# Performance work log

Measured on AMD Instinct MI355X. Metric: run time of the kernel, lower is better.

The kernel has to match this reference:

```python
import jax, jax.numpy as jnp
import numpy as np

TOP_K = 8


def setup_inputs() -> dict:
    key = jax.random.key(0)
    k1, k2 = jax.random.split(key)
    B, S, D, E = 4, 4096, 2048, 64
    x = jax.random.normal(k1, (B, S, D), dtype=jnp.float32)
    # nn.Linear(d_model, n_experts): weight [E, D], bias [E]
    W = jax.random.normal(k2, (E, D), dtype=jnp.float32) * (1.0 / np.sqrt(D))
    b = jnp.zeros((E,), dtype=jnp.float32)
    return {"x": x, "W": W, "b": b}


def reference(x, W, b):
    # logits: [B, S, E] = x @ W^T + b
    logits = jnp.einsum("bsd,ed->bse", x, W) + b
    scores = jax.nn.sigmoid(logits)                      # [B, S, E]
    B, S, E = scores.shape
    flat = scores.reshape(B * S, E)                      # tokens x experts
    top_w, top_idx = jax.lax.top_k(flat, TOP_K)          # [B*S, k]
    return top_w.reshape(B, S, TOP_K), top_idx.reshape(B, S, TOP_K)
```

## Files before the change

kernel.cpp:

```cpp
#include <hip/hip_runtime.h>
#include <math.h>

#define TOKENS 16384
#define DMODEL 2048
#define NEXP   64
#define TOPK   8
#define BM     64
#define BK     32
#define PAD    4

__global__ __launch_bounds__(256) void router_gemm(
    const float* __restrict__ x, const float* __restrict__ W,
    float* __restrict__ part, int kchunk)
{
    __shared__ float xsT[BK][BM + PAD];
    __shared__ float wsT[BK][NEXP + PAD];

    const int tid = threadIdx.x;
    const int kq  = tid & 7;
    const int row = tid >> 3;
    const int ty  = tid >> 4;
    const int tx  = tid & 15;
    const size_t tokBase = (size_t)blockIdx.x * BM;
    const int    kc      = blockIdx.y;
    const size_t kbase   = (size_t)kc * (size_t)kchunk;

    double accd[4][4];
    float  accf[4][4];
#pragma unroll
    for (int i = 0; i < 4; ++i)
#pragma unroll
        for (int j = 0; j < 4; ++j) { accd[i][j] = 0.0; accf[i][j] = 0.0f; }

    for (int k0 = 0; k0 < kchunk; k0 += BK) {
        const size_t koff = kbase + (size_t)k0 + kq * 4;
        const float4 xa = *(const float4*)(x + (tokBase + row) * DMODEL + koff);
        const float4 xb = *(const float4*)(x + (tokBase + row + 32) * DMODEL + koff);
        const float4 wa = *(const float4*)(W + (size_t)row * DMODEL + koff);
        const float4 wb = *(const float4*)(W + (size_t)(row + 32) * DMODEL + koff);
        __syncthreads();
        xsT[kq * 4 + 0][row] = xa.x; xsT[kq * 4 + 1][row] = xa.y;
        xsT[kq * 4 + 2][row] = xa.z; xsT[kq * 4 + 3][row] = xa.w;
        xsT[kq * 4 + 0][row + 32] = xb.x; xsT[kq * 4 + 1][row + 32] = xb.y;
        xsT[kq * 4 + 2][row + 32] = xb.z; xsT[kq * 4 + 3][row + 32] = xb.w;
        wsT[kq * 4 + 0][row] = wa.x; wsT[kq * 4 + 1][row] = wa.y;
        wsT[kq * 4 + 2][row] = wa.z; wsT[kq * 4 + 3][row] = wa.w;
        wsT[kq * 4 + 0][row + 32] = wb.x; wsT[kq * 4 + 1][row + 32] = wb.y;
        wsT[kq * 4 + 2][row + 32] = wb.z; wsT[kq * 4 + 3][row + 32] = wb.w;
        __syncthreads();

#pragma unroll
        for (int kk = 0; kk < BK; ++kk) {
            const float4 a = *(const float4*)(&xsT[kk][ty * 4]);
            const float4 b = *(const float4*)(&wsT[kk][tx * 4]);
            const float av[4] = {a.x, a.y, a.z, a.w};
            const float bv[4] = {b.x, b.y, b.z, b.w};
#pragma unroll
            for (int i = 0; i < 4; ++i)
#pragma unroll
                for (int j = 0; j < 4; ++j)
                    accf[i][j] = fmaf(av[i], bv[j], accf[i][j]);
            if ((kk & 15) == 15) {
#pragma unroll
                for (int i = 0; i < 4; ++i)
#pragma unroll
                    for (int j = 0; j < 4; ++j) {
                        accd[i][j] += (double)accf[i][j];
                        accf[i][j] = 0.0f;
                    }
            }
        }
    }

#pragma unroll
    for (int i = 0; i < 4; ++i) {
        const size_t tok = tokBase + ty * 4 + i;
        float4 o;
        o.x = (float)accd[i][0]; o.y = (float)accd[i][1];
        o.z = (float)accd[i][2]; o.w = (float)accd[i][3];
        *(float4*)(part + ((size_t)kc * TOKENS + tok) * NEXP + tx * 4) = o;
    }
}

__global__ __launch_bounds__(256) void router_reduce_topk(
    const float* __restrict__ part, const float* __restrict__ bias,
    float* __restrict__ out_w, float* __restrict__ out_i, int ksplit)
{
    const int lane = threadIdx.x & 63;
    const int wid  = threadIdx.x >> 6;
    const size_t t = (size_t)blockIdx.x * 4 + wid;

    double vd = (double)bias[lane];
    for (int kc = 0; kc < ksplit; ++kc)
        vd += (double)part[((size_t)kc * TOKENS + t) * NEXP + lane];
    float v = (float)vd;

    const int myi = lane;
    float bv = 0.0f; int bi = 0;
#pragma unroll
    for (int r = 0; r < TOPK; ++r) {
        float mv = v; int mi = myi;
#pragma unroll
        for (int off = 32; off > 0; off >>= 1) {
            const float ov = __shfl_xor(mv, off, 64);
            const int   oi = __shfl_xor(mi, off, 64);
            if (ov > mv || (ov == mv && oi < mi)) { mv = ov; mi = oi; }
        }
        if (lane == r)  { bv = mv; bi = mi; }
        if (myi == mi)  { v = -INFINITY; }
    }

    if (lane < TOPK) {
        out_w[t * TOPK + lane] = 1.0f / (1.0f + expf(-bv));
        out_i[t * TOPK + lane] = (float)bi;
    }
}

extern "C" void kernel_launch(void* const* d_in, const int* in_sizes, int n_in,
                              void* d_out, int out_size, void* d_ws, size_t ws_size,
                              hipStream_t stream) {
    const float* x    = (const float*)d_in[0];
    const float* W    = (const float*)d_in[1];
    const float* bias = (const float*)d_in[2];
    float* out_w = (float*)d_out;
    float* out_i = (float*)d_out + (size_t)TOKENS * TOPK;
    float* part  = (float*)d_ws;

    const size_t per = (size_t)TOKENS * NEXP * sizeof(float);
    int ksplit = 8;
    while (ksplit > 1 && ws_size < (size_t)ksplit * per) ksplit >>= 1;
    const int kchunk = DMODEL / ksplit;

    dim3 grid(TOKENS / BM, ksplit);
    router_gemm<<<grid, 256, 0, stream>>>(x, W, part, kchunk);
    router_reduce_topk<<<TOKENS / 4, 256, 0, stream>>>(part, bias, out_w, out_i, ksplit);
}
```

Baseline: 234.6 us.

## Prefetch next K tile into registers and store shared tiles row-major with float4

Shared tiles are now stored k-contiguous per row, so each thread writes one float4 instead of sixteen scalar transposed stores. The inner product reads four float4 per operand per 4-k group. The next tile's global loads are issued right after the barrier, so they overlap with the FMA loop on the current tile. In exchange the kernel holds more live registers, and the row-major float4 reads with a 36-float stride may cause LDS bank conflicts.

Result: slower. 284.8 us (+21.4%).

```diff
diff --git a/kernel.cpp b/kernel.cpp
--- a/kernel.cpp
+++ b/kernel.cpp
@@ -7,14 +7,14 @@
 #define TOPK   8
 #define BM     64
 #define BK     32
-#define PAD    4
+#define BKP    36
 
 __global__ __launch_bounds__(256) void router_gemm(
     const float* __restrict__ x, const float* __restrict__ W,
     float* __restrict__ part, int kchunk)
 {
-    __shared__ float xsT[BK][BM + PAD];
-    __shared__ float wsT[BK][NEXP + PAD];
+    __shared__ float xs[BM][BKP];
+    __shared__ float ws[NEXP][BKP];
 
     const int tid = threadIdx.x;
     const int kq  = tid & 7;
@@ -32,35 +32,47 @@
 #pragma unroll
         for (int j = 0; j < 4; ++j) { accd[i][j] = 0.0; accf[i][j] = 0.0f; }
 
-    for (int k0 = 0; k0 < kchunk; k0 += BK) {
-        const size_t koff = kbase + (size_t)k0 + kq * 4;
-        const float4 xa = *(const float4*)(x + (tokBase + row) * DMODEL + koff);
-        const float4 xb = *(const float4*)(x + (tokBase + row + 32) * DMODEL + koff);
-        const float4 wa = *(const float4*)(W + (size_t)row * DMODEL + koff);
-        const float4 wb = *(const float4*)(W + (size_t)(row + 32) * DMODEL + koff);
+    const int ntiles = kchunk / BK;
+
+    size_t koff = kbase + kq * 4;
+    float4 xa = *(const float4*)(x + (tokBase + row) * DMODEL + koff);
+    float4 xb = *(const float4*)(x + (tokBase + row + 32) * DMODEL + koff);
+    float4 wa = *(const float4*)(W + (size_t)row * DMODEL + koff);
+    float4 wb = *(const float4*)(W + (size_t)(row + 32) * DMODEL + koff);
+
+    for (int t = 0; t < ntiles; ++t) {
         __syncthreads();
-        xsT[kq * 4 + 0][row] = xa.x; xsT[kq * 4 + 1][row] = xa.y;
-        xsT[kq * 4 + 2][row] = xa.z; xsT[kq * 4 + 3][row] = xa.w;
-        xsT[kq * 4 + 0][row + 32] = xb.x; xsT[kq * 4 + 1][row + 32] = xb.y;
-        xsT[kq * 4 + 2][row + 32] = xb.z; xsT[kq * 4 + 3][row + 32] = xb.w;
-        wsT[kq * 4 + 0][row] = wa.x; wsT[kq * 4 + 1][row] = wa.y;
-        wsT[kq * 4 + 2][row] = wa.z; wsT[kq * 4 + 3][row] = wa.w;
-        wsT[kq * 4 + 0][row + 32] = wb.x; wsT[kq * 4 + 1][row + 32] = wb.y;
-        wsT[kq * 4 + 2][row + 32] = wb.z; wsT[kq * 4 + 3][row + 32] = wb.w;
+        *(float4*)(&xs[row     ][kq * 4]) = xa;
+        *(float4*)(&xs[row + 32][kq * 4]) = xb;
+        *(float4*)(&ws[row     ][kq * 4]) = wa;
+        *(float4*)(&ws[row + 32][kq * 4]) = wb;
         __syncthreads();
 
+        if (t + 1 < ntiles) {
+            koff = kbase + (size_t)(t + 1) * BK + kq * 4;
+            xa = *(const float4*)(x + (tokBase + row) * DMODEL + koff);
+            xb = *(const float4*)(x + (tokBase + row + 32) * DMODEL + koff);
+            wa = *(const float4*)(W + (size_t)row * DMODEL + koff);
+            wb = *(const float4*)(W + (size_t)(row + 32) * DMODEL + koff);
+        }
+
 #pragma unroll
-        for (int kk = 0; kk < BK; ++kk) {
-            const float4 a = *(const float4*)(&xsT[kk][ty * 4]);
-            const float4 b = *(const float4*)(&wsT[kk][tx * 4]);
-            const float av[4] = {a.x, a.y, a.z, a.w};
-            const float bv[4] = {b.x, b.y, b.z, b.w};
+        for (int g = 0; g < BK / 4; ++g) {
+            float a[16], b[16];
 #pragma unroll
             for (int i = 0; i < 4; ++i)
+                *(float4*)(&a[i * 4]) = *(const float4*)(&xs[ty * 4 + i][g * 4]);
 #pragma unroll
-                for (int j = 0; j < 4; ++j)
-                    accf[i][j] = fmaf(av[i], bv[j], accf[i][j]);
-            if ((kk & 15) == 15) {
+            for (int j = 0; j < 4; ++j)
+                *(float4*)(&b[j * 4]) = *(const float4*)(&ws[tx * 4 + j][g * 4]);
+#pragma unroll
+            for (int c = 0; c < 4; ++c)
+#pragma unroll
+                for (int i = 0; i < 4; ++i)
+#pragma unroll
+                    for (int j = 0; j < 4; ++j)
+                        accf[i][j] = fmaf(a[i * 4 + c], b[j * 4 + c], accf[i][j]);
+            if ((g & 3) == 3) {
 #pragma unroll
                 for (int i = 0; i < 4; ++i)
 #pragma unroll
```

## Read x directly from global memory and prefetch W tiles into registers

Applied to the files above, without the earlier changes.

The x tile is no longer staged through shared memory. Each thread now loads its own four token rows straight from global memory as float4, and only W is kept in LDS. The next W tile is loaded into registers while the current tile is computed, and the double-precision flush now happens once per 32-wide k tile instead of every 16. This removes LDS write traffic for x and overlaps the W global loads with compute, but x is now fetched redundantly by the 16 threads sharing a ty row, which relies on cache hits. The longer fp32 partial sum also changes numerical accumulation slightly.

After: 279.7 us. 19.2% more time.

```diff
diff --git a/kernel.cpp b/kernel.cpp
--- a/kernel.cpp
+++ b/kernel.cpp
@@ -7,14 +7,13 @@
 #define TOPK   8
 #define BM     64
 #define BK     32
-#define PAD    4
+#define WPAD   4
 
 __global__ __launch_bounds__(256) void router_gemm(
     const float* __restrict__ x, const float* __restrict__ W,
     float* __restrict__ part, int kchunk)
 {
-    __shared__ float xsT[BK][BM + PAD];
-    __shared__ float wsT[BK][NEXP + PAD];
+    __shared__ float wsT[BK][NEXP + WPAD];
 
     const int tid = threadIdx.x;
     const int kq  = tid & 7;
@@ -25,6 +24,11 @@
     const int    kc      = blockIdx.y;
     const size_t kbase   = (size_t)kc * (size_t)kchunk;
 
+    const float* xr0 = x + (tokBase + ty * 4 + 0) * DMODEL + kbase;
+    const float* xr1 = x + (tokBase + ty * 4 + 1) * DMODEL + kbase;
+    const float* xr2 = x + (tokBase + ty * 4 + 2) * DMODEL + kbase;
+    const float* xr3 = x + (tokBase + ty * 4 + 3) * DMODEL + kbase;
+
     double accd[4][4];
     float  accf[4][4];
 #pragma unroll
@@ -32,44 +36,60 @@
 #pragma unroll
         for (int j = 0; j < 4; ++j) { accd[i][j] = 0.0; accf[i][j] = 0.0f; }
 
-    for (int k0 = 0; k0 < kchunk; k0 += BK) {
-        const size_t koff = kbase + (size_t)k0 + kq * 4;
-        const float4 xa = *(const float4*)(x + (tokBase + row) * DMODEL + koff);
-        const float4 xb = *(const float4*)(x + (tokBase + row + 32) * DMODEL + koff);
-        const float4 wa = *(const float4*)(W + (size_t)row * DMODEL + koff);
-        const float4 wb = *(const float4*)(W + (size_t)(row + 32) * DMODEL + koff);
+    const int ntiles = kchunk / BK;
+
+    const float* wp = W + (size_t)row * DMODEL + kbase + kq * 4;
+    float4 wa = *(const float4*)(wp);
+    float4 wb = *(const float4*)(wp + (size_t)32 * DMODEL);
+
+    for (int t = 0; t < ntiles; ++t) {
         __syncthreads();
-        xsT[kq * 4 + 0][row] = xa.x; xsT[kq * 4 + 1][row] = xa.y;
-        xsT[kq * 4 + 2][row] = xa.z; xsT[kq * 4 + 3][row] = xa.w;
-        xsT[kq * 4 + 0][row + 32] = xb.x; xsT[kq * 4 + 1][row + 32] = xb.y;
-        xsT[kq * 4 + 2][row + 32] = xb.z; xsT[kq * 4 + 3][row + 32] = xb.w;
         wsT[kq * 4 + 0][row] = wa.x; wsT[kq * 4 + 1][row] = wa.y;
         wsT[kq * 4 + 2][row] = wa.z; wsT[kq * 4 + 3][row] = wa.w;
         wsT[kq * 4 + 0][row + 32] = wb.x; wsT[kq * 4 + 1][row + 32] = wb.y;
         wsT[kq * 4 + 2][row + 32] = wb.z; wsT[kq * 4 + 3][row + 32] = wb.w;
         __syncthreads();
 
+        if (t + 1 < ntiles) {
+            wp += BK;
+            wa = *(const float4*)(wp);
+            wb = *(const float4*)(wp + (size_t)32 * DMODEL);
+        }
+
+        const int kb = t * BK;
 #pragma unroll
-        for (int kk = 0; kk < BK; ++kk) {
-            const float4 a = *(const float4*)(&xsT[kk][ty * 4]);
-            const float4 b = *(const float4*)(&wsT[kk][tx * 4]);
-            const float av[4] = {a.x, a.y, a.z, a.w};
-            const float bv[4] = {b.x, b.y, b.z, b.w};
+        for (int g = 0; g < BK / 4; ++g) {
+            float4 xv0 = *(const float4*)(xr0 + kb + g * 4);
+            float4 xv1 = *(const float4*)(xr1 + kb + g * 4);
+            float4 xv2 = *(const float4*)(xr2 + kb + g * 4);
+            float4 xv3 = *(const float4*)(xr3 + kb + g * 4);
+            float4 b0 = *(const float4*)(&wsT[g * 4 + 0][tx * 4]);
+            float4 b1 = *(const float4*)(&wsT[g * 4 + 1][tx * 4]);
+            float4 b2 = *(const float4*)(&wsT[g * 4 + 2][tx * 4]);
+            float4 b3 = *(const float4*)(&wsT[g * 4 + 3][tx * 4]);
+            const float a[4][4] = {{xv0.x, xv0.y, xv0.z, xv0.w},
+                                   {xv1.x, xv1.y, xv1.z, xv1.w},
+                                   {xv2.x, xv2.y, xv2.z, xv2.w},
+                                   {xv3.x, xv3.y, xv3.z, xv3.w}};
+            const float b[4][4] = {{b0.x, b0.y, b0.z, b0.w},
+                                   {b1.x, b1.y, b1.z, b1.w},
+                                   {b2.x, b2.y, b2.z, b2.w},
+                                   {b3.x, b3.y, b3.z, b3.w}};
 #pragma unroll
-            for (int i = 0; i < 4; ++i)
-#pragma unroll
-                for (int j = 0; j < 4; ++j)
-                    accf[i][j] = fmaf(av[i], bv[j], accf[i][j]);
-            if ((kk & 15) == 15) {
+            for (int c = 0; c < 4; ++c)
 #pragma unroll
                 for (int i = 0; i < 4; ++i)
 #pragma unroll
-                    for (int j = 0; j < 4; ++j) {
-                        accd[i][j] += (double)accf[i][j];
-                        accf[i][j] = 0.0f;
-                    }
+                    for (int j = 0; j < 4; ++j)
+                        accf[i][j] = fmaf(a[i][c], b[c][j], accf[i][j]);
+        }
+#pragma unroll
+        for (int i = 0; i < 4; ++i)
+#pragma unroll
+            for (int j = 0; j < 4; ++j) {
+                accd[i][j] += (double)accf[i][j];
+                accf[i][j] = 0.0f;
             }
-        }
     }
 
 #pragma unroll
```

## Replace FP32 SIMT router GEMM with split-fp16 MFMA using pre-swizzled weights

Applied to the files above, without the earlier changes.

Moves the router GEMM from scalar FMA on LDS tiles to 16x16x32 fp16 MFMA instructions. Each operand is split into high and low fp16 halves, and three MFMAs per step approximate fp32 accuracy. A new kernel converts W into the split fp16 form in MFMA fragment order, and x is read directly from global memory without LDS staging. The split-K factor is fixed at 4. The workspace size check is dropped, and there is some risk of top-k mismatches from reduced precision and fp16 range limits on the low parts.

New measurement: 232.1 us. No clear change (-1.0%).

```diff
diff --git a/kernel.cpp b/kernel.cpp
--- a/kernel.cpp
+++ b/kernel.cpp
@@ -5,80 +5,100 @@
 #define DMODEL 2048
 #define NEXP   64
 #define TOPK   8
-#define BM     64
-#define BK     32
-#define PAD    4
+#define KSPLIT 4
+#define KCHUNK (DMODEL / KSPLIT)
+#define NKS    (KCHUNK / 32)
 
-__global__ __launch_bounds__(256) void router_gemm(
-    const float* __restrict__ x, const float* __restrict__ W,
-    float* __restrict__ part, int kchunk)
+typedef _Float16 half8 __attribute__((ext_vector_type(8)));
+typedef float    f32x4 __attribute__((ext_vector_type(4)));
+
+
+__global__ __launch_bounds__(64) void w_convert(
+    const float* __restrict__ W, _Float16* __restrict__ wh,
+    _Float16* __restrict__ wl)
 {
-    __shared__ float xsT[BK][BM + PAD];
-    __shared__ float wsT[BK][NEXP + PAD];
+    const int lane = threadIdx.x;
+    const int nt   = blockIdx.x & 3;
+    const int ks   = blockIdx.x >> 2;
+    const int n    = nt * 16 + (lane & 15);
+    const int k0   = ks * 32 + (lane >> 4) * 8;
+    const size_t base = ((size_t)(nt * 64 + ks) * 64 + lane) * 8;
+#pragma unroll
+    for (int j = 0; j < 8; ++j) {
+        const float w = W[(size_t)n * DMODEL + k0 + j];
+        const _Float16 h = (_Float16)w;
+        wh[base + j] = h;
+        wl[base + j] = (_Float16)(w - (float)h);
+    }
+}
 
-    const int tid = threadIdx.x;
-    const int kq  = tid & 7;
-    const int row = tid >> 3;
-    const int ty  = tid >> 4;
-    const int tx  = tid & 15;
-    const size_t tokBase = (size_t)blockIdx.x * BM;
-    const int    kc      = blockIdx.y;
-    const size_t kbase   = (size_t)kc * (size_t)kchunk;
+__global__ __launch_bounds__(256) void router_gemm_mfma(
+    const float* __restrict__ x, const _Float16* __restrict__ wh,
+    const _Float16* __restrict__ wl, float* __restrict__ part)
+{
+    const int lane = threadIdx.x & 63;
+    const int wid  = threadIdx.x >> 6;
+    const int kc   = blockIdx.y;
+    const size_t tokBase = (size_t)blockIdx.x * 64 + wid * 16;
+    const int m    = lane & 15;
+    const int quad = lane >> 4;
 
-    double accd[4][4];
-    float  accf[4][4];
+    const float* xrow = x + (tokBase + m) * DMODEL + (size_t)kc * KCHUNK + quad * 8;
+
+    f32x4 C[4];
+    double accd[16];
 #pragma unroll
-    for (int i = 0; i < 4; ++i)
+    for (int nt = 0; nt < 4; ++nt) { C[nt] = (f32x4)0.0f; }
 #pragma unroll
-        for (int j = 0; j < 4; ++j) { accd[i][j] = 0.0; accf[i][j] = 0.0f; }
+    for (int i = 0; i < 16; ++i) accd[i] = 0.0;
 
-    for (int k0 = 0; k0 < kchunk; k0 += BK) {
-        const size_t koff = kbase + (size_t)k0 + kq * 4;
-        const float4 xa = *(const float4*)(x + (tokBase + row) * DMODEL + koff);
-        const float4 xb = *(const float4*)(x + (tokBase + row + 32) * DMODEL + koff);
-        const float4 wa = *(const float4*)(W + (size_t)row * DMODEL + koff);
-        const float4 wb = *(const float4*)(W + (size_t)(row + 32) * DMODEL + koff);
-        __syncthreads();
-        xsT[kq * 4 + 0][row] = xa.x; xsT[kq * 4 + 1][row] = xa.y;
-        xsT[kq * 4 + 2][row] = xa.z; xsT[kq * 4 + 3][row] = xa.w;
-        xsT[kq * 4 + 0][row + 32] = xb.x; xsT[kq * 4 + 1][row + 32] = xb.y;
-        xsT[kq * 4 + 2][row + 32] = xb.z; xsT[kq * 4 + 3][row + 32] = xb.w;
-        wsT[kq * 4 + 0][row] = wa.x; wsT[kq * 4 + 1][row] = wa.y;
-        wsT[kq * 4 + 2][row] = wa.z; wsT[kq * 4 + 3][row] = wa.w;
-        wsT[kq * 4 + 0][row + 32] = wb.x; wsT[kq * 4 + 1][row + 32] = wb.y;
-        wsT[kq * 4 + 2][row + 32] = wb.z; wsT[kq * 4 + 3][row + 32] = wb.w;
-        __syncthreads();
+    for (int ks = 0; ks < NKS; ++ks) {
+        float xv[8];
+        *(float4*)(&xv[0]) = *(const float4*)(xrow + ks * 32);
+        *(float4*)(&xv[4]) = *(const float4*)(xrow + ks * 32 + 4);
+        half8 ah, al;
+#pragma unroll
+        for (int j = 0; j < 8; ++j) {
+            const _Float16 h = (_Float16)xv[j];
+            ah[j] = h;
+            al[j] = (_Float16)(xv[j] - (float)h);
+        }
+        const int gks = kc * NKS + ks;
+        half8 bh[4], bl[4];
+#pragma unroll
+        for (int nt = 0; nt < 4; ++nt) {
+            const size_t fb = ((size_t)(nt * 64 + gks) * 64 + lane) * 8;
+            bh[nt] = *(const half8*)(wh + fb);
+            bl[nt] = *(const half8*)(wl + fb);
+        }
+#pragma unroll
+        for (int nt = 0; nt < 4; ++nt)
+            C[nt] = __builtin_amdgcn_mfma_f32_16x16x32_f16(ah, bh[nt], C[nt], 0, 0, 0);
+#pragma unroll
+        for (int nt = 0; nt < 4; ++nt)
+            C[nt] = __builtin_amdgcn_mfma_f32_16x16x32_f16(al, bh[nt], C[nt], 0, 0, 0);
+#pragma unroll
+        for (int nt = 0; nt < 4; ++nt)
+            C[nt] = __builtin_amdgcn_mfma_f32_16x16x32_f16(ah, bl[nt], C[nt], 0, 0, 0);
 
+        if ((ks & 3) == 3) {
 #pragma unroll
-        for (int kk = 0; kk < BK; ++kk) {
-            const float4 a = *(const float4*)(&xsT[kk][ty * 4]);
-            const float4 b = *(const float4*)(&wsT[kk][tx * 4]);
-            const float av[4] = {a.x, a.y, a.z, a.w};
-            const float bv[4] = {b.x, b.y, b.z, b.w};
+            for (int nt = 0; nt < 4; ++nt) {
 #pragma unroll
-            for (int i = 0; i < 4; ++i)
-#pragma unroll
-                for (int j = 0; j < 4; ++j)
-                    accf[i][j] = fmaf(av[i], bv[j], accf[i][j]);
-            if ((kk & 15) == 15) {
-#pragma unroll
-                for (int i = 0; i < 4; ++i)
-#pragma unroll
-                    for (int j = 0; j < 4; ++j) {
-                        accd[i][j] += (double)accf[i][j];
-                        accf[i][j] = 0.0f;
-                    }
+                for (int r = 0; r < 4; ++r) accd[nt * 4 + r] += (double)C[nt][r];
+                C[nt] = (f32x4)0.0f;
             }
         }
     }
 
 #pragma unroll
-    for (int i = 0; i < 4; ++i) {
-        const size_t tok = tokBase + ty * 4 + i;
-        float4 o;
-        o.x = (float)accd[i][0]; o.y = (float)accd[i][1];
-        o.z = (float)accd[i][2]; o.w = (float)accd[i][3];
-        *(float4*)(part + ((size_t)kc * TOKENS + tok) * NEXP + tx * 4) = o;
+    for (int r = 0; r < 4; ++r) {
+        const size_t tok = tokBase + quad * 4 + r;
+#pragma unroll
+        for (int nt = 0; nt < 4; ++nt) {
+            part[((size_t)kc * TOKENS + tok) * NEXP + nt * 16 + m] =
+                (float)accd[nt * 4 + r];
+        }
     }
 }
 
@@ -124,14 +144,14 @@
     const float* bias = (const float*)d_in[2];
     float* out_w = (float*)d_out;
     float* out_i = (float*)d_out + (size_t)TOKENS * TOPK;
-    float* part  = (float*)d_ws;
 
-    const size_t per = (size_t)TOKENS * NEXP * sizeof(float);
-    int ksplit = 8;
-    while (ksplit > 1 && ws_size < (size_t)ksplit * per) ksplit >>= 1;
-    const int kchunk = DMODEL / ksplit;
+    float*    part = (float*)d_ws;
+    _Float16* wh   = (_Float16*)((char*)d_ws +
+                       (size_t)KSPLIT * TOKENS * NEXP * sizeof(float));
+    _Float16* wl   = wh + (size_t)NEXP * DMODEL;
 
-    dim3 grid(TOKENS / BM, ksplit);
-    router_gemm<<<grid, 256, 0, stream>>>(x, W, part, kchunk);
-    router_reduce_topk<<<TOKENS / 4, 256, 0, stream>>>(part, bias, out_w, out_i, ksplit);
+    w_convert<<<256, 64, 0, stream>>>(W, wh, wl);
+    dim3 grid(TOKENS / 64, KSPLIT);
+    router_gemm_mfma<<<grid, 256, 0, stream>>>(x, wh, wl, part);
+    router_reduce_topk<<<TOKENS / 4, 256, 0, stream>>>(part, bias, out_w, out_i, KSPLIT);
 }
```
